# Kernel tuning notes

Measured on AMD Instinct MI355X. Metric: run time of the kernel, lower is better.

The kernel has to match this reference:

```python
import jax, jax.numpy as jnp
import numpy as np

TAU = 3.0          # CPG tau
VTH = 1.0          # LIF v_threshold (v_reset = 0, hard reset)
PEAK = 16          # peak population size
NUM_E = 25         # int(32 * 0.8) excitatory neurons
FATIGUE_TH = 8
ALPHA = 4.0        # spikingjelly sigmoid surrogate alpha (unused in fwd)


def spike_fn(x):
    # Heaviside threshold at 0 (v >= VTH fires)
    return (x >= 0.0).astype(x.dtype)


def setup_inputs() -> dict:
    key = jax.random.key(0)
    k0, k1, k2, k3, k4 = jax.random.split(key, 5)
    B, N = 524288, 32
    spike_history = (jax.random.uniform(k0, (B, N)) < 0.3).astype(jnp.float32)
    neighbor_E_spikes = (jax.random.uniform(k1, (B, 8, NUM_E)) < 0.3).astype(jnp.float32)
    # mutual_inhibition: -2.0 everywhere, within-population blocks *0.1 -> -0.2,
    # cross-population blocks set to -3.0
    is_peak = jnp.arange(N) < PEAK
    same_pop = is_peak[:, None] == is_peak[None, :]
    mutual_inhibition = jnp.where(same_pop, -0.2, -3.0).astype(jnp.float32)
    coupling_W = jax.random.normal(k2, (N, NUM_E), dtype=jnp.float32) * 0.2
    peak_fatigue = jax.random.randint(k3, (B,), 0, 10, dtype=jnp.int32)
    trough_fatigue = jax.random.randint(k4, (B,), 0, 10, dtype=jnp.int32)
    v0 = jnp.zeros((B, N), dtype=jnp.float32)
    return {
        "spike_history": spike_history,
        "neighbor_E_spikes": neighbor_E_spikes,
        "mutual_inhibition": mutual_inhibition,
        "coupling_W": coupling_W,
        "v0": v0,
        "peak_fatigue": peak_fatigue,
        "trough_fatigue": trough_fatigue,
        "num_ticks": 5,
    }


def reference(spike_history, neighbor_E_spikes, mutual_inhibition, coupling_W,
              v0, peak_fatigue, trough_fatigue, num_ticks):
    B = spike_history.shape[0]
    # fatigue-driven drive: trough fatigue excites peak half, peak fatigue excites trough half
    dp = jnp.where(trough_fatigue >= FATIGUE_TH, 2.0, 0.0)[:, None]  # [B,1]
    dt = jnp.where(peak_fatigue >= FATIGUE_TH, 2.0, 0.0)[:, None]
    drive = jnp.concatenate(
        [jnp.broadcast_to(dp, (B, PEAK)), jnp.broadcast_to(dt, (B, 32 - PEAK))], axis=-1)
    # neighbor coupling: sum_k W @ nbr_k ; constant across ticks, hoisted out of loop
    coupling = jnp.einsum('bkn,mn->bm', neighbor_E_spikes, coupling_W)
    base = drive + 0.3 * coupling  # [B,32]

    def step(carry, _):
        v, sh, acc = carry
        recurrent = jnp.einsum('bn,mn->bm', sh, mutual_inhibition)  # sh @ M.T
        x = base + 0.5 * recurrent
        # LIF (decay_input=True): v += (x - (v - v_reset)) / tau, v_reset = 0
        v = v + (x - v) / TAU
        s = spike_fn(v - VTH)
        v = v * (1.0 - s)  # hard reset to 0
        return (v, s, acc + s), None

    init = (v0, spike_history, jnp.zeros_like(v0))
    (v, sh, acc), _ = jax.lax.scan(step, init, None, length=num_ticks)
    should_stay = acc[:, PEAK:].sum(axis=-1) > 0.5  # trough active => STAY
    return acc[:, :NUM_E], should_stay
```

## Files before the change

### kernel.cpp

```cpp
#include <hip/hip_runtime.h>


#define FATIGUE_TH 8

__global__ __launch_bounds__(256) void AgentLSM_70841190580507_kernel(
    const float* __restrict__ sh_in,
    const float* __restrict__ nbr,
    const float* __restrict__ M,
    const float* __restrict__ W,
    const int*   __restrict__ pf,
    const int*   __restrict__ tf,
    const int*   __restrict__ ticks_p,
    float* __restrict__ out_acc,
    float* __restrict__ out_stay,
    int B)
{
    __shared__ float4 lds_nbr4[400];
    __shared__ float4 lds_W4[200];
    __shared__ float  lds_cnt[8 * 33];
    __shared__ float  lds_out[200];
    __shared__ float  lds_stay[8];

    float* lds_nbr = (float*)lds_nbr4;
    float* lds_W   = (float*)lds_W4;

    const int tid = threadIdx.x;
    const int g   = tid >> 5;
    const int m   = tid & 31;
    const long long b = (long long)blockIdx.x * 8 + g;
    const bool valid = (b < (long long)B);
    const int nv = min(8, B - blockIdx.x * 8);

    if (tid < 200) lds_W4[tid] = ((const float4*)W)[tid];

    {
        const long long fbase = (long long)blockIdx.x * 1600;
        const long long ftot  = (long long)B * 200;
        const float4* nb4 = (const float4*)nbr;
        #pragma unroll
        for (int i = tid; i < 400; i += 256) {
            long long f0 = fbase + (long long)i * 4;
            lds_nbr4[i] = (f0 + 3 < ftot) ? nb4[fbase / 4 + i]
                                          : make_float4(0.f, 0.f, 0.f, 0.f);
        }
    }
    __syncthreads();

    if (m < 25) {
        float c = 0.f;
        #pragma unroll
        for (int k = 0; k < 8; ++k) c += lds_nbr[g * 200 + k * 25 + m];
        lds_cnt[g * 33 + m] = c;
    }
    __syncthreads();

    float coup = 0.f;
    #pragma unroll
    for (int n = 0; n < 25; ++n)
        coup += lds_cnt[g * 33 + n] * lds_W[m * 25 + n];

    const float a_same  = M[0];
    const float a_cross = M[16];

    float drive = 0.f;
    int init_bit = 0;
    if (valid) {
        drive = (m < 16) ? ((tf[b] >= FATIGUE_TH) ? 2.0f : 0.0f)
                         : ((pf[b] >= FATIGUE_TH) ? 2.0f : 0.0f);
        init_bit = (sh_in[b * 32 + m] != 0.0f);
    }
    float base = drive + 0.3f * coup;
    float v = 0.0f;

    unsigned long long bal = __ballot(init_bit);
    unsigned int mask = (unsigned int)(bal >> (tid & 32));

    const int T = ticks_p[0];
    int acc = 0;
    unsigned int any_tr = 0;
    const bool is_peak = (m < 16);

    #define TICK()  do {                                                   \
        float Spf = (float)__popc(mask & 0xFFFFu);                         \
        float Stf = (float)__popc(mask >> 16);                             \
        float rec = is_peak ? (a_same * Spf + a_cross * Stf)               \
                            : (a_cross * Spf + a_same * Stf);              \
        float x = base + 0.5f * rec;                                       \
        v = v + (x - v) / 3.0f;                  \
        bool s = (v >= 1.0f);                 \
        unsigned long long sb = __ballot(s);                               \
        mask = (unsigned int)(sb >> (tid & 32));                           \
        any_tr |= (mask >> 16);                                            \
        acc += s ? 1 : 0;                                                  \
        v = s ? 0.0f : v;                                                  \
    } while (0)

    if (T == 5) {
        TICK(); TICK(); TICK(); TICK(); TICK();
    } else {
        for (int t = 0; t < T; ++t) TICK();
    }
    #undef TICK

    if (m < 25) lds_out[g * 25 + m] = (float)acc;
    if (m == 31) lds_stay[g] = any_tr ? 1.0f : 0.0f;
    __syncthreads();

    const long long obase = (long long)blockIdx.x * 200;
    if (nv == 8) {
        if (tid < 50)
            ((float4*)out_acc)[obase / 4 + tid] =
                ((const float4*)lds_out)[tid];
        if (tid < 8)
            out_stay[(long long)blockIdx.x * 8 + tid] = lds_stay[tid];
    } else {
        if (tid < nv * 25) out_acc[obase + tid] = lds_out[tid];
        if (tid < nv)      out_stay[(long long)blockIdx.x * 8 + tid] = lds_stay[tid];
    }
}

extern "C" void kernel_launch(void* const* d_in, const int* in_sizes, int n_in,
                              void* d_out, int out_size, void* d_ws, size_t ws_size,
                              hipStream_t stream) {
    const float* sh    = (const float*)d_in[0];
    const float* nbr   = (const float*)d_in[1];
    const float* M     = (const float*)d_in[2];
    const float* W     = (const float*)d_in[3];
    const int*   pf    = (const int*)d_in[5];
    const int*   tf    = (const int*)d_in[6];
    const int*   ticks = (const int*)d_in[7];

    const int B = in_sizes[5];
    float* out_acc  = (float*)d_out;
    float* out_stay = out_acc + (long long)B * 25;

    const int blocks = (B + 7) / 8;
    AgentLSM_70841190580507_kernel<<<blocks, 256, 0, stream>>>(
        sh, nbr, M, W, pf, tf, ticks, out_acc, out_stay, B);
}
```

Baseline: 639.7 us.

## Use persistent grid-stride blocks and keep coupling weights in registers

The launch now uses at most 2048 persistent blocks that loop over 8-agent chunks instead of one block per chunk. Each thread loads its row of the coupling matrix into registers once, and the per-agent neighbor counts are read back from LDS as float4. This is meant to cut per-block launch and W-staging overhead and reduce LDS traffic. In exchange it adds register pressure and a loop that does not overlap loads across chunks, which may reduce the memory parallelism available for this bandwidth-bound kernel.

New measurement: 680.7 us. +6.4%, slower.

```diff
diff --git a/kernel.cpp b/kernel.cpp
--- a/kernel.cpp
+++ b/kernel.cpp
@@ -13,109 +13,126 @@
     const int*   __restrict__ ticks_p,
     float* __restrict__ out_acc,
     float* __restrict__ out_stay,
-    int B)
+    int B, int nchunks)
 {
     __shared__ float4 lds_nbr4[400];
-    __shared__ float4 lds_W4[200];
-    __shared__ float  lds_cnt[8 * 33];
+    __shared__ float  lds_cnt[8 * 28];
     __shared__ float  lds_out[200];
     __shared__ float  lds_stay[8];
 
     float* lds_nbr = (float*)lds_nbr4;
-    float* lds_W   = (float*)lds_W4;
 
     const int tid = threadIdx.x;
     const int g   = tid >> 5;
     const int m   = tid & 31;
-    const long long b = (long long)blockIdx.x * 8 + g;
-    const bool valid = (b < (long long)B);
-    const int nv = min(8, B - blockIdx.x * 8);
+    const bool is_peak = (m < 16);
 
-    if (tid < 200) lds_W4[tid] = ((const float4*)W)[tid];
-
-    {
-        const long long fbase = (long long)blockIdx.x * 1600;
-        const long long ftot  = (long long)B * 200;
-        const float4* nb4 = (const float4*)nbr;
-        #pragma unroll
-        for (int i = tid; i < 400; i += 256) {
-            long long f0 = fbase + (long long)i * 4;
-            lds_nbr4[i] = (f0 + 3 < ftot) ? nb4[fbase / 4 + i]
-                                          : make_float4(0.f, 0.f, 0.f, 0.f);
-        }
-    }
-    __syncthreads();
-
-    if (m < 25) {
-        float c = 0.f;
-        #pragma unroll
-        for (int k = 0; k < 8; ++k) c += lds_nbr[g * 200 + k * 25 + m];
-        lds_cnt[g * 33 + m] = c;
-    }
-    __syncthreads();
-
-    float coup = 0.f;
+    float w[28];
     #pragma unroll
-    for (int n = 0; n < 25; ++n)
-        coup += lds_cnt[g * 33 + n] * lds_W[m * 25 + n];
+    for (int n = 0; n < 25; ++n) w[n] = W[m * 25 + n];
+    w[25] = 0.f; w[26] = 0.f; w[27] = 0.f;
 
     const float a_same  = M[0];
     const float a_cross = M[16];
+    const int T = ticks_p[0];
 
-    float drive = 0.f;
-    int init_bit = 0;
-    if (valid) {
-        drive = (m < 16) ? ((tf[b] >= FATIGUE_TH) ? 2.0f : 0.0f)
-                         : ((pf[b] >= FATIGUE_TH) ? 2.0f : 0.0f);
-        init_bit = (sh_in[b * 32 + m] != 0.0f);
-    }
-    float base = drive + 0.3f * coup;
-    float v = 0.0f;
+    for (int chunk = blockIdx.x; chunk < nchunks; chunk += gridDim.x) {
+        const long long b = (long long)chunk * 8 + g;
+        const int nv = min(8, B - chunk * 8);
+        const bool valid = (g < nv);
 
-    unsigned long long bal = __ballot(init_bit);
-    unsigned int mask = (unsigned int)(bal >> (tid & 32));
+        const float4* nb4 = (const float4*)nbr + (long long)chunk * 400;
+        if (nv == 8) {
+            #pragma unroll
+            for (int i = tid; i < 400; i += 256) lds_nbr4[i] = nb4[i];
+        } else {
+            const long long ftot  = (long long)B * 200;
+            const long long fbase = (long long)chunk * 1600;
+            for (int i = tid; i < 400; i += 256) {
+                long long f0 = fbase + (long long)i * 4;
+                lds_nbr4[i] = (f0 + 3 < ftot) ? nb4[i]
+                                              : make_float4(0.f, 0.f, 0.f, 0.f);
+            }
+        }
 
-    const int T = ticks_p[0];
-    int acc = 0;
-    unsigned int any_tr = 0;
-    const bool is_peak = (m < 16);
+        float drive = 0.f;
+        int init_bit = 0;
+        if (valid) {
+            drive = is_peak ? ((tf[b] >= FATIGUE_TH) ? 2.0f : 0.0f)
+                            : ((pf[b] >= FATIGUE_TH) ? 2.0f : 0.0f);
+            init_bit = (sh_in[b * 32 + m] != 0.0f);
+        }
 
-    #define TICK()  do {                                                   \
-        float Spf = (float)__popc(mask & 0xFFFFu);                         \
-        float Stf = (float)__popc(mask >> 16);                             \
-        float rec = is_peak ? (a_same * Spf + a_cross * Stf)               \
-                            : (a_cross * Spf + a_same * Stf);              \
-        float x = base + 0.5f * rec;                                       \
-        v = v + (x - v) / 3.0f;                  \
-        bool s = (v >= 1.0f);                 \
-        unsigned long long sb = __ballot(s);                               \
-        mask = (unsigned int)(sb >> (tid & 32));                           \
-        any_tr |= (mask >> 16);                                            \
-        acc += s ? 1 : 0;                                                  \
-        v = s ? 0.0f : v;                                                  \
-    } while (0)
+        __syncthreads();
 
-    if (T == 5) {
-        TICK(); TICK(); TICK(); TICK(); TICK();
-    } else {
-        for (int t = 0; t < T; ++t) TICK();
-    }
-    #undef TICK
+        if (m < 28) {
+            float c = 0.f;
+            if (m < 25) {
+                #pragma unroll
+                for (int k = 0; k < 8; ++k) c += lds_nbr[g * 200 + k * 25 + m];
+            }
+            lds_cnt[g * 28 + m] = c;
+        }
 
-    if (m < 25) lds_out[g * 25 + m] = (float)acc;
-    if (m == 31) lds_stay[g] = any_tr ? 1.0f : 0.0f;
-    __syncthreads();
+        __syncthreads();
 
-    const long long obase = (long long)blockIdx.x * 200;
-    if (nv == 8) {
-        if (tid < 50)
-            ((float4*)out_acc)[obase / 4 + tid] =
-                ((const float4*)lds_out)[tid];
-        if (tid < 8)
-            out_stay[(long long)blockIdx.x * 8 + tid] = lds_stay[tid];
-    } else {
-        if (tid < nv * 25) out_acc[obase + tid] = lds_out[tid];
-        if (tid < nv)      out_stay[(long long)blockIdx.x * 8 + tid] = lds_stay[tid];
+        float coup = 0.f;
+        {
+            const float4* c4p = (const float4*)&lds_cnt[g * 28];
+            #pragma unroll
+            for (int q = 0; q < 7; ++q) {
+                float4 c4 = c4p[q];
+                coup += c4.x * w[4*q+0] + c4.y * w[4*q+1]
+                      + c4.z * w[4*q+2] + c4.w * w[4*q+3];
+            }
+        }
+
+        const float base = drive + 0.3f * coup;
+        float v = 0.0f;
+
+        unsigned long long bal = __ballot(init_bit);
+        unsigned int mask = (unsigned int)(bal >> (tid & 32));
+
+        int acc = 0;
+        unsigned int any_tr = 0;
+
+        #define TICK()  do {                                                   \
+            float Spf = (float)__popc(mask & 0xFFFFu);                         \
+            float Stf = (float)__popc(mask >> 16);                             \
+            float rec = is_peak ? (a_same * Spf + a_cross * Stf)               \
+                                : (a_cross * Spf + a_same * Stf);              \
+            float x = base + 0.5f * rec;                                       \
+            v = v + (x - v) / 3.0f;                  \
+            bool s = (v >= 1.0f);                 \
+            unsigned long long sb = __ballot(s);                               \
+            mask = (unsigned int)(sb >> (tid & 32));                           \
+            any_tr |= (mask >> 16);                                            \
+            acc += s ? 1 : 0;                                                  \
+            v = s ? 0.0f : v;                                                  \
+        } while (0)
+
+        if (T == 5) {
+            TICK(); TICK(); TICK(); TICK(); TICK();
+        } else {
+            for (int t = 0; t < T; ++t) TICK();
+        }
+        #undef TICK
+
+        if (m < 25) lds_out[g * 25 + m] = (float)acc;
+        if (m == 31) lds_stay[g] = any_tr ? 1.0f : 0.0f;
+        __syncthreads();
+
+        const long long obase = (long long)chunk * 200;
+        if (nv == 8) {
+            if (tid < 50)
+                ((float4*)out_acc)[obase / 4 + tid] =
+                    ((const float4*)lds_out)[tid];
+            if (tid < 8)
+                out_stay[(long long)chunk * 8 + tid] = lds_stay[tid];
+        } else {
+            if (tid < nv * 25) out_acc[obase + tid] = lds_out[tid];
+            if (tid < nv)      out_stay[(long long)chunk * 8 + tid] = lds_stay[tid];
+        }
     }
 }
 
@@ -134,7 +151,8 @@
     float* out_acc  = (float*)d_out;
     float* out_stay = out_acc + (long long)B * 25;
 
-    const int blocks = (B + 7) / 8;
+    const int nchunks = (B + 7) / 8;
+    int blocks = nchunks < 2048 ? nchunks : 2048;
     AgentLSM_70841190580507_kernel<<<blocks, 256, 0, stream>>>(
-        sh, nbr, M, W, pf, tf, ticks, out_acc, out_stay, B);
+        sh, nbr, M, W, pf, tf, ticks, out_acc, out_stay, B, nchunks);
 }
```
